# Performance work log

Measured on AMD Instinct MI355X. Metric: run time of the kernel, lower is better.

The kernel has to match this reference:

```python
import jax, jax.numpy as jnp
import numpy as np

EPS = 1e-5
INF = 1e9
H, D = 16, 24  # no_heads, c_hidden

def layer_norm(x, w, b):
    mu = jnp.mean(x, axis=-1, keepdims=True)
    var = jnp.mean(jnp.square(x - mu), axis=-1, keepdims=True)
    return (x - mu) * jax.lax.rsqrt(var + EPS) * w + b

def setup_inputs() -> dict:
    key = jax.random.key(0)
    ks = jax.random.split(key, 12)
    B, N, Cq, Cz = 1, 1024, 384, 128
    s = 0.02
    return {
        "a": jax.random.normal(ks[0], (B, N, Cq), jnp.float32),
        "z": jax.random.normal(ks[1], (B, N, N, Cz), jnp.float32),
        "mask": jnp.ones((B, N), jnp.float32),
        "ln_a_w": jnp.ones((Cq,), jnp.float32),
        "ln_a_b": jnp.zeros((Cq,), jnp.float32),
        "ln_z_w": jnp.ones((Cz,), jnp.float32),
        "ln_z_b": jnp.zeros((Cz,), jnp.float32),
        "w_z": jax.random.normal(ks[2], (Cz, H), jnp.float32) * s,
        "wq": jax.random.normal(ks[3], (Cq, H * D), jnp.float32) * s,
        "wk": jax.random.normal(ks[4], (Cq, H * D), jnp.float32) * s,
        "wv": jax.random.normal(ks[5], (Cq, H * D), jnp.float32) * s,
        "wg": jax.random.normal(ks[6], (Cq, H * D), jnp.float32) * s,
        "bg": jnp.ones((H * D,), jnp.float32),
        "wo": jax.random.normal(ks[7], (H * D, Cq), jnp.float32) * s,
        "bo": jnp.zeros((Cq,), jnp.float32),
    }

def reference(a, z, mask, ln_a_w, ln_a_b, ln_z_w, ln_z_b, w_z, wq, wk, wv, wg, bg, wo, bo):
    B, N, Cq = a.shape
    a_ln = layer_norm(a, ln_a_w, ln_a_b)                      # [B,N,Cq]
    # pair bias: LN -> Linear(no bias) -> permute to [B,H,N,N]
    zb = layer_norm(z, ln_z_w, ln_z_b) @ w_z                  # [B,N,N,H]
    pair_bias = jnp.transpose(zb, (0, 3, 1, 2))               # [B,H,N,N]
    mask_bias = (INF * (mask - 1.0))[:, None, None, :]        # [B,1,1,N]
    q = (a_ln @ wq).reshape(B, N, H, D) * (D ** -0.5)
    k = (a_ln @ wk).reshape(B, N, H, D)
    v = (a_ln @ wv).reshape(B, N, H, D)
    logits = jnp.einsum("bqhd,bkhd->bhqk", q, k) + mask_bias + pair_bias
    attn = jax.nn.softmax(logits, axis=-1)
    o = jnp.einsum("bhqk,bkhd->bqhd", attn, v)                # [B,N,H,D]
    g = jax.nn.sigmoid(a_ln @ wg + bg).reshape(B, N, H, D)
    o = (g * o).reshape(B, N, H * D)
    return o @ wo + bo
```

## Files before the change

### kernel.cpp

```cpp
#include <hip/hip_runtime.h>
#include <hip/hip_bf16.h>

typedef float f32x4 __attribute__((ext_vector_type(4)));
typedef short s16x8 __attribute__((ext_vector_type(8)));

__device__ __forceinline__ unsigned short f2bf(float x){
  unsigned u = __float_as_uint(x);
  u += 0x7fffu + ((u >> 16) & 1u);
  return (unsigned short)(u >> 16);
}
__device__ __forceinline__ float bf2f(unsigned short h){
  return __uint_as_float(((unsigned)h) << 16);
}
__device__ __forceinline__ unsigned pk_bf(float a, float b){
  __hip_bfloat162 t = __float22bfloat162_rn(make_float2(a, b));
  return *reinterpret_cast<unsigned*>(&t);
}

__global__ __launch_bounds__(256) void prep_kernel(const float* __restrict__ a, const float* __restrict__ ln_a_w,
                             const float* __restrict__ ln_a_b, const float* __restrict__ lnzw,
                             const float* __restrict__ lnzb, const float* __restrict__ w_z,
                             const float* __restrict__ wq, const float* __restrict__ wk,
                             const float* __restrict__ wv, const float* __restrict__ wg,
                             const float* __restrict__ wo,
                             unsigned short* __restrict__ a_lnB, unsigned short* __restrict__ wBall,
                             unsigned short* __restrict__ wwB, float* __restrict__ TU,
                             unsigned short* __restrict__ qTp, unsigned short* __restrict__ kTp,
                             unsigned short* __restrict__ vTt){
  int bid = blockIdx.x, tid = threadIdx.x;
  if (bid < 180){
    __shared__ float t[64][65];
    int mat = bid/36, tt = bid - mat*36;
    int c0 = (tt % 6)*64, k0 = (tt / 6)*64;
    const float* src = mat == 0 ? wq : mat == 1 ? wk : mat == 2 ? wv : mat == 3 ? wg : wo;
    int r = tid >> 4, c4 = (tid & 15)*4;
    #pragma unroll
    for (int rr = 0; rr < 4; ++rr){
      float4 v = *(const float4*)(src + (size_t)(k0 + r + rr*16)*384 + c0 + c4);
      t[r + rr*16][c4+0] = v.x; t[r + rr*16][c4+1] = v.y;
      t[r + rr*16][c4+2] = v.z; t[r + rr*16][c4+3] = v.w;
    }
    __syncthreads();
    float scale = (mat == 0) ? 0.20412414523193154f : 1.f;
    int cc = tid >> 2, kp = (tid & 3)*16;
    unsigned ow[8];
    #pragma unroll
    for (int j = 0; j < 8; ++j)
      ow[j] = pk_bf(t[kp + 2*j][cc]*scale, t[kp + 2*j + 1][cc]*scale);
    unsigned short* dst = wBall + ((size_t)(mat*384 + c0 + cc)*384 + k0 + kp);
    *(uint4*)dst       = make_uint4(ow[0], ow[1], ow[2], ow[3]);
    *(uint4*)(dst + 8) = make_uint4(ow[4], ow[5], ow[6], ow[7]);
  } else if (bid < 436){
    int r = (bid - 180)*4 + (tid >> 6), l = tid & 63;
    const float* ap = a + (size_t)r*384;
    float x[6]; float s = 0.f, sq = 0.f;
    #pragma unroll
    for (int i = 0; i < 6; ++i){ x[i] = ap[i*64 + l]; s += x[i]; sq += x[i]*x[i]; }
    #pragma unroll
    for (int off = 32; off; off >>= 1){ s += __shfl_xor(s, off); sq += __shfl_xor(sq, off); }
    float mu = s*(1.f/384.f);
    float var = sq*(1.f/384.f) - mu*mu;
    float rs = rsqrtf(var + 1e-5f);
    #pragma unroll
    for (int i = 0; i < 6; ++i){ int c = i*64 + l; a_lnB[(size_t)r*384 + c] = f2bf((x[i]-mu)*rs*ln_a_w[c] + ln_a_b[c]); }
  } else if (bid == 436){
    if (tid < 128){
      float lw = lnzw[tid];
      #pragma unroll
      for (int h = 0; h < 16; ++h) wwB[tid*16 + h] = f2bf(lw * w_z[tid*16 + h]);
    }
    if (tid < 16){
      float T = 0.f, U = 0.f;
      for (int c = 0; c < 128; ++c){ T += lnzw[c]*w_z[c*16 + tid]; U += lnzb[c]*w_z[c*16 + tid]; }
      TU[tid] = T; TU[16 + tid] = U;
    }
  } else {
    int t = (bid - 437)*256 + tid;
    uint4 zv = make_uint4(0,0,0,0);
    if (t < 16384)      *(uint4*)(qTp + (size_t)t*32 + 24) = zv;
    else if (t < 32768) *(uint4*)(kTp + (size_t)(t - 16384)*32 + 24) = zv;
    else {
      int t2 = t - 32768;
      int h = t2 >> 10, w = t2 & 1023;
      *(uint4*)(vTt + ((size_t)h*32 + 24)*1024 + (size_t)w*8) = zv;
    }
  }
}

__global__ __launch_bounds__(256) void qkvg_kernel(const unsigned short* __restrict__ AB,
                                                   const unsigned short* __restrict__ wBt,
                                                   const float* __restrict__ bg,
                                                   unsigned short* __restrict__ qTp, unsigned short* __restrict__ kTp,
                                                   unsigned short* __restrict__ vTt, float* __restrict__ g){
  __shared__ short Al[64*8*8];
  __shared__ short Bl[64*8*8];
  int tid = threadIdx.x;
  int wave = tid >> 6, lane = tid & 63, l15 = lane & 15, sub = lane >> 4;
  int n0 = blockIdx.x*64, m0 = blockIdx.y*64;
  f32x4 acc[4];
  #pragma unroll
  for (int c = 0; c < 4; ++c) acc[c] = (f32x4){0.f,0.f,0.f,0.f};
  const s16x8* Ag = (const s16x8*)AB;
  const s16x8* Bg = (const s16x8*)wBt;
  s16x8* Al8 = (s16x8*)Al; s16x8* Bl8 = (s16x8*)Bl;
  for (int ks = 0; ks < 6; ++ks){
    int k0u = ks*8;
    #pragma unroll
    for (int j = 0; j < 2; ++j){
      int idx = tid*2 + j;
      int row = idx >> 3, u = idx & 7;
      Al8[row*8 + (u ^ (row & 7))] = Ag[(size_t)(m0 + row)*48 + k0u + u];
      Bl8[row*8 + (u ^ (row & 7))] = Bg[(size_t)(n0 + row)*48 + k0u + u];
    }
    __syncthreads();
    #pragma unroll
    for (int kk = 0; kk < 2; ++kk){
      int arow = wave*16 + l15;
      s16x8 af = Al8[arow*8 + ((kk*4 + sub) ^ (arow & 7))];
      #pragma unroll
      for (int c = 0; c < 4; ++c){
        int brow = c*16 + l15;
        s16x8 bf = Bl8[brow*8 + ((kk*4 + sub) ^ (brow & 7))];
        acc[c] = __builtin_amdgcn_mfma_f32_16x16x32_bf16(af, bf, acc[c], 0, 0, 0);
      }
    }
    __syncthreads();
  }
  int which = blockIdx.x / 6;
  int cb = n0 - which*384;
  if (which == 3){
    #pragma unroll
    for (int c = 0; c < 4; ++c){
      int col = cb + c*16 + l15;
      #pragma unroll
      for (int r = 0; r < 4; ++r){
        int row = m0 + wave*16 + sub*4 + r;
        float t = acc[c][r] + bg[col];
        g[(size_t)row*384 + col] = 1.f/(1.f + __expf(-t));
      }
    }
  } else if (which == 2){
    #pragma unroll
    for (int c = 0; c < 4; ++c){
      int col = cb + c*16 + l15;
      int h = col/24, d = col - h*24;
      unsigned p0 = pk_bf(acc[c][0], acc[c][1]);
      unsigned p1 = pk_bf(acc[c][2], acc[c][3]);
      size_t base = ((size_t)h*32 + d)*1024 + (size_t)(m0 + wave*16 + sub*4);
      *(uint2*)(vTt + base) = make_uint2(p0, p1);
    }
  } else {
    unsigned short* dst = which == 0 ? qTp : kTp;
    #pragma unroll
    for (int c = 0; c < 4; ++c){
      int col = cb + c*16 + l15;
      int h = col/24, d = col - h*24;
      #pragma unroll
      for (int r = 0; r < 4; ++r){
        int row = m0 + wave*16 + sub*4 + r;
        dst[((size_t)(h << 10) + row)*32 + d] = f2bf(acc[c][r]);
      }
    }
  }
}

__global__ __launch_bounds__(256) void zbias_kernel(const float* __restrict__ z, const unsigned short* __restrict__ wwB,
                                                    const float* __restrict__ TU, const float* __restrict__ mask,
                                                    unsigned short* __restrict__ pbM){
  __shared__ float sums[2][64];
  __shared__ float sqs[2][64];
  __shared__ float accT[2][64][17];
  int tid = threadIdx.x;
  int wave = tid >> 6, lane = tid & 63;
  int h = lane & 15, sub = lane >> 4;
  s16x8 bfr[4];
  #pragma unroll
  for (int kc = 0; kc < 4; ++kc)
    #pragma unroll
    for (int j = 0; j < 8; ++j) bfr[kc][j] = (short)wwB[(kc*32 + sub*8 + j)*16 + h];
  s16x8 ones1;
  #pragma unroll
  for (int j = 0; j < 8; ++j) ones1[j] = (h == 0) ? (short)0x3F80 : (short)0;
  int eh = tid >> 4, ej = tid & 15;
  float Te = TU[eh], Ue = TU[16 + eh];
  for (int it = 0; it < 4; ++it){
    int bb = it & 1;
    int tile = blockIdx.x + it*4096;
    int qt = tile >> 6, kt = tile & 63;
    int q0 = qt*4, k0 = kt*16;
    const float* zrow = z + ((size_t)(q0 + wave)*1024 + k0 + h)*128;
    f32x4 acc  = {0.f, 0.f, 0.f, 0.f};
    f32x4 accS = {0.f, 0.f, 0.f, 0.f};
    f32x4 accG = {0.f, 0.f, 0.f, 0.f};
    #pragma unroll
    for (int kc = 0; kc < 4; ++kc){
      f32x4 v0 = *(const f32x4*)(zrow + kc*32 + sub*8);
      f32x4 v1 = *(const f32x4*)(zrow + kc*32 + sub*8 + 4);
      union { unsigned u[4]; s16x8 s; } cv;
      cv.u[0] = pk_bf(v0.x, v0.y); cv.u[1] = pk_bf(v0.z, v0.w);
      cv.u[2] = pk_bf(v1.x, v1.y); cv.u[3] = pk_bf(v1.z, v1.w);
      s16x8 af = cv.s;
      acc  = __builtin_amdgcn_mfma_f32_16x16x32_bf16(af, bfr[kc], acc, 0, 0, 0);
      accS = __builtin_amdgcn_mfma_f32_16x16x32_bf16(af, ones1, accS, 0, 0, 0);
      accG = __builtin_amdgcn_mfma_f32_16x16x32_bf16(af, af, accG, 0, 0, 0);
    }
    #pragma unroll
    for (int r = 0; r < 4; ++r) accT[bb][wave*16 + sub*4 + r][h] = acc[r];
    if (h == 0){
      #pragma unroll
      for (int r = 0; r < 4; ++r) sums[bb][wave*16 + sub*4 + r] = accS[r];
    }
    if (sub == (h >> 2)){
      int r = h & 3;
      float vq = r == 0 ? accG[0] : r == 1 ? accG[1] : r == 2 ? accG[2] : accG[3];
      sqs[bb][wave*16 + h] = vq;
    }
    __syncthreads();
    int k = k0 + ej;
    float mb = 1e9f*(mask[k] - 1.f);
    unsigned short pv[4];
    #pragma unroll
    for (int i = 0; i < 4; ++i){
      int row = i*16 + ej;
      float mu = sums[bb][row]*(1.f/128.f);
      float var = sqs[bb][row]*(1.f/128.f) - mu*mu;
      float rs = rsqrtf(var + 1e-5f);
      pv[i] = f2bf(rs*(accT[bb][row][eh] - mu*Te) + Ue + mb);
    }
    int qb = q0 >> 6, qg = (q0 >> 4) & 3, subq = (q0 >> 2) & 3;
    int kkt = k >> 6, c = (k >> 4) & 3, l15k = k & 15;
    size_t off = ((((size_t)(eh*16 + qb)*16 + kkt)*4 + qg)*4 + c)*256 + (size_t)(subq*16 + l15k)*4;
    *(uint2*)(pbM + off) = make_uint2(((unsigned)pv[1] << 16) | pv[0], ((unsigned)pv[3] << 16) | pv[2]);
  }
}

__global__ __launch_bounds__(512) void attn_kernel(const unsigned short* __restrict__ qTp, const unsigned short* __restrict__ kTp,
                                                   const unsigned short* __restrict__ vTt, const unsigned short* __restrict__ pbM,
                                                   const float* __restrict__ g, unsigned short* __restrict__ ogB){
  __shared__ float lds[8192];
  int tid = threadIdx.x;
  int wave = tid >> 6, lane = tid & 63, l15 = lane & 15, sub = lane >> 4;
  int qb32 = blockIdx.x, h = blockIdx.y;
  int qg_l = wave & 1, kkq = wave >> 1;
  int qrow = qb32*32 + qg_l*16 + l15;
  int qb64 = qb32 >> 1, qg4 = (qb32 & 1)*2 + qg_l;
  const unsigned short* kBase = kTp + ((size_t)(h << 10))*32;
  const unsigned short* vBase = vTt + (size_t)h*32*1024;
  const unsigned short* pbW = pbM + (size_t)(h*16 + qb64)*16*4096 + (size_t)qg4*1024 + (size_t)lane*4;
  uint2 pvAll[4][4];
  #pragma unroll
  for (int t = 0; t < 4; ++t){
    const unsigned short* pbt = pbW + (size_t)(kkq*4 + t)*4096;
    pvAll[t][0] = *(const uint2*)(pbt + 0);
    pvAll[t][1] = *(const uint2*)(pbt + 256);
    pvAll[t][2] = *(const uint2*)(pbt + 512);
    pvAll[t][3] = *(const uint2*)(pbt + 768);
  }
  s16x8 qf = *(const s16x8*)(qTp + ((size_t)(h << 10) + qrow)*32 + sub*8);
  f32x4 o0 = {0.f,0.f,0.f,0.f}, o1 = {0.f,0.f,0.f,0.f};
  float m[4] = {-1e30f,-1e30f,-1e30f,-1e30f}, l[4] = {0.f,0.f,0.f,0.f};
  char* Pb = (char*)(lds + wave*1024);
  s16x8 kfA0, kfA1, kfA2, kfA3;
  {
    int kk0 = (kkq*4)*64;
    kfA0 = *(const s16x8*)(kBase + (size_t)(kk0 +  0 + l15)*32 + sub*8);
    kfA1 = *(const s16x8*)(kBase + (size_t)(kk0 + 16 + l15)*32 + sub*8);
    kfA2 = *(const s16x8*)(kBase + (size_t)(kk0 + 32 + l15)*32 + sub*8);
    kfA3 = *(const s16x8*)(kBase + (size_t)(kk0 + 48 + l15)*32 + sub*8);
  }
  #pragma unroll
  for (int t = 0; t < 4; ++t){
    int kkt = kkq*4 + t;
    int kk0 = kkt*64;
    f32x4 s[4];
    s[0] = __builtin_amdgcn_mfma_f32_16x16x32_bf16(qf, kfA0, (f32x4){0.f,0.f,0.f,0.f}, 0, 0, 0);
    s[1] = __builtin_amdgcn_mfma_f32_16x16x32_bf16(qf, kfA1, (f32x4){0.f,0.f,0.f,0.f}, 0, 0, 0);
    s[2] = __builtin_amdgcn_mfma_f32_16x16x32_bf16(qf, kfA2, (f32x4){0.f,0.f,0.f,0.f}, 0, 0, 0);
    s[3] = __builtin_amdgcn_mfma_f32_16x16x32_bf16(qf, kfA3, (f32x4){0.f,0.f,0.f,0.f}, 0, 0, 0);
    if (t < 3){
      int nk = kk0 + 64;
      kfA0 = *(const s16x8*)(kBase + (size_t)(nk +  0 + l15)*32 + sub*8);
      kfA1 = *(const s16x8*)(kBase + (size_t)(nk + 16 + l15)*32 + sub*8);
      kfA2 = *(const s16x8*)(kBase + (size_t)(nk + 32 + l15)*32 + sub*8);
      kfA3 = *(const s16x8*)(kBase + (size_t)(nk + 48 + l15)*32 + sub*8);
    }
    #pragma unroll
    for (int c = 0; c < 4; ++c){
      s[c][0] += bf2f((unsigned short)(pvAll[t][c].x & 0xffff));
      s[c][1] += bf2f((unsigned short)(pvAll[t][c].x >> 16));
      s[c][2] += bf2f((unsigned short)(pvAll[t][c].y & 0xffff));
      s[c][3] += bf2f((unsigned short)(pvAll[t][c].y >> 16));
    }
    #pragma unroll
    for (int r = 0; r < 4; ++r){
      float pm = fmaxf(fmaxf(s[0][r], s[1][r]), fmaxf(s[2][r], s[3][r]));
      pm = fmaxf(pm, __shfl_xor(pm, 1));
      pm = fmaxf(pm, __shfl_xor(pm, 2));
      pm = fmaxf(pm, __shfl_xor(pm, 4));
      pm = fmaxf(pm, __shfl_xor(pm, 8));
      float mn = fmaxf(m[r], pm);
      float corr = __expf(m[r] - mn);
      m[r] = mn;
      float ps = 0.f;
      #pragma unroll
      for (int c = 0; c < 4; ++c){ s[c][r] = __expf(s[c][r] - mn); ps += s[c][r]; }
      ps += __shfl_xor(ps, 1); ps += __shfl_xor(ps, 2);
      ps += __shfl_xor(ps, 4); ps += __shfl_xor(ps, 8);
      l[r] = l[r]*corr + ps;
      o0[r] *= corr; o1[r] *= corr;
    }
    #pragma unroll
    for (int c = 0; c < 4; ++c){
      #pragma unroll
      for (int r = 0; r < 4; ++r){
        int qq = sub*4 + r;
        int byte = ((qq*128 + (c*16 + l15)*2)) ^ ((qq & 7) << 4);
        *(short*)(Pb + byte) = (short)f2bf(s[c][r]);
      }
    }
    #pragma unroll
    for (int kh = 0; kh < 2; ++kh){
      int byteA = (l15*128 + kh*64 + sub*16) ^ ((l15 & 7) << 4);
      s16x8 pa = *(const s16x8*)(Pb + byteA);
      s16x8 vb0 = *(const s16x8*)(vBase + (size_t)l15*1024 + kk0 + kh*32 + sub*8);
      s16x8 vb1 = *(const s16x8*)(vBase + (size_t)(16 + l15)*1024 + kk0 + kh*32 + sub*8);
      o0 = __builtin_amdgcn_mfma_f32_16x16x32_bf16(pa, vb0, o0, 0, 0, 0);
      o1 = __builtin_amdgcn_mfma_f32_16x16x32_bf16(pa, vb1, o1, 0, 0, 0);
    }
  }
  {
    float* cw = lds + wave*1024 + lane*16;
    cw[0] = o0[0]; cw[1] = o0[1]; cw[2] = o0[2]; cw[3] = o0[3];
    cw[4] = o1[0]; cw[5] = o1[1]; cw[6] = o1[2]; cw[7] = o1[3];
    cw[8] = m[0]; cw[9] = m[1]; cw[10] = m[2]; cw[11] = m[3];
    cw[12] = l[0]; cw[13] = l[1]; cw[14] = l[2]; cw[15] = l[3];
  }
  __syncthreads();
  if (kkq == 0){
    #pragma unroll
    for (int k2 = 1; k2 < 4; ++k2){
      const float* c2 = lds + (size_t)(k2*2 + qg_l)*1024 + lane*16;
      #pragma unroll
      for (int r = 0; r < 4; ++r){
        float m2 = c2[8 + r], l2 = c2[12 + r];
        float nm = fmaxf(m[r], m2);
        float f1 = __expf(m[r] - nm), f2 = __expf(m2 - nm);
        l[r] = l[r]*f1 + l2*f2;
        o0[r] = o0[r]*f1 + c2[r]*f2;
        o1[r] = o1[r]*f1 + c2[4 + r]*f2;
        m[r] = nm;
      }
    }
    #pragma unroll
    for (int r = 0; r < 4; ++r){
      float inv = 1.f/l[r];
      int q = qb32*32 + qg_l*16 + sub*4 + r;
      size_t base = (size_t)q*384 + h*24;
      ogB[base + l15] = f2bf(g[base + l15]*o0[r]*inv);
      if (l15 < 8) ogB[base + 16 + l15] = f2bf(g[base + 16 + l15]*o1[r]*inv);
    }
  }
}

__global__ __launch_bounds__(256) void gemm_out(const unsigned short* __restrict__ AB,
                                                const unsigned short* __restrict__ wBo,
                                                const float* __restrict__ bo, float* __restrict__ dst){
  __shared__ short Al[64*8*8];
  __shared__ short Bl[64*8*8];
  int tid = threadIdx.x;
  int wave = tid >> 6, lane = tid & 63, l15 = lane & 15, sub = lane >> 4;
  int n0 = blockIdx.x*64, m0 = blockIdx.y*64;
  f32x4 acc[4];
  #pragma unroll
  for (int c = 0; c < 4; ++c) acc[c] = (f32x4){0.f,0.f,0.f,0.f};
  const s16x8* Ag = (const s16x8*)AB;
  const s16x8* Bg = (const s16x8*)wBo;
  s16x8* Al8 = (s16x8*)Al; s16x8* Bl8 = (s16x8*)Bl;
  for (int ks = 0; ks < 6; ++ks){
    int k0u = ks*8;
    #pragma unroll
    for (int j = 0; j < 2; ++j){
      int idx = tid*2 + j;
      int row = idx >> 3, u = idx & 7;
      Al8[row*8 + (u ^ (row & 7))] = Ag[(size_t)(m0 + row)*48 + k0u + u];
      Bl8[row*8 + (u ^ (row & 7))] = Bg[(size_t)(n0 + row)*48 + k0u + u];
    }
    __syncthreads();
    #pragma unroll
    for (int kk = 0; kk < 2; ++kk){
      int arow = wave*16 + l15;
      s16x8 af = Al8[arow*8 + ((kk*4 + sub) ^ (arow & 7))];
      #pragma unroll
      for (int c = 0; c < 4; ++c){
        int brow = c*16 + l15;
        s16x8 bf = Bl8[brow*8 + ((kk*4 + sub) ^ (brow & 7))];
        acc[c] = __builtin_amdgcn_mfma_f32_16x16x32_bf16(af, bf, acc[c], 0, 0, 0);
      }
    }
    __syncthreads();
  }
  #pragma unroll
  for (int c = 0; c < 4; ++c){
    int col = n0 + c*16 + l15;
    float b = bo[col];
    #pragma unroll
    for (int r = 0; r < 4; ++r){
      int row = m0 + wave*16 + sub*4 + r;
      dst[(size_t)row*384 + col] = acc[c][r] + b;
    }
  }
}

extern "C" void kernel_launch(void* const* d_in, const int* in_sizes, int n_in,
                              void* d_out, int out_size, void* d_ws, size_t ws_size,
                              hipStream_t stream){
  const float* a      = (const float*)d_in[0];
  const float* z      = (const float*)d_in[1];
  const float* mask   = (const float*)d_in[2];
  const float* ln_a_w = (const float*)d_in[3];
  const float* ln_a_b = (const float*)d_in[4];
  const float* ln_z_w = (const float*)d_in[5];
  const float* ln_z_b = (const float*)d_in[6];
  const float* w_z    = (const float*)d_in[7];
  const float* wq     = (const float*)d_in[8];
  const float* wk     = (const float*)d_in[9];
  const float* wv     = (const float*)d_in[10];
  const float* wg     = (const float*)d_in[11];
  const float* bg     = (const float*)d_in[12];
  const float* wo     = (const float*)d_in[13];
  const float* bo     = (const float*)d_in[14];

  char* ws = (char*)d_ws;
  unsigned short* a_lnB = (unsigned short*)(ws + ((size_t)0u));
  unsigned short* wBall = (unsigned short*)(ws + ((size_t)1u << 20));
  unsigned short* qTp   = (unsigned short*)(ws + ((size_t)4u << 20));
  unsigned short* kTp   = (unsigned short*)(ws + ((size_t)6u << 20));
  unsigned short* vTt   = (unsigned short*)(ws + ((size_t)8u << 20));
  float* g    = (float*)(ws + ((size_t)10u << 20));
  unsigned short* ogB = (unsigned short*)(ws + ((size_t)12u << 20));
  unsigned short* wwB = (unsigned short*)(ws + ((size_t)14u << 20));
  float* TU   = (float*)(ws + ((size_t)14u << 20) + 8192);
  unsigned short* pbM = (unsigned short*)(ws + ((size_t)24u << 20));

  hipLaunchKernelGGL(prep_kernel, dim3(629), dim3(256), 0, stream, a, ln_a_w, ln_a_b,
                     ln_z_w, ln_z_b, w_z, wq, wk, wv, wg, wo, a_lnB, wBall, wwB, TU, qTp, kTp, vTt);
  hipLaunchKernelGGL(qkvg_kernel, dim3(24,16), dim3(256), 0, stream, a_lnB, wBall, bg, qTp, kTp, vTt, g);
  hipLaunchKernelGGL(zbias_kernel, dim3(4096), dim3(256), 0, stream, z, wwB, TU, mask, pbM);
  hipLaunchKernelGGL(attn_kernel, dim3(32,16), dim3(512), 0, stream, qTp, kTp, vTt, pbM, g, ogB);
  hipLaunchKernelGGL(gemm_out, dim3(6,16), dim3(256), 0, stream, ogB, wBall + (size_t)4*384*384, bo, (float*)d_out);
}
```

Baseline: 159.0 us.

## Transpose QK^T MFMA so softmax rows lie along lanes, retile pair-bias layout

The attention kernel swaps the MFMA operands so each lane holds scores for a single query across keys. The row max and sum then need only two cross-lane shuffles instead of four per row, and the P tile is written to LDS as packed 8-byte stores rather than individual shorts. The pair-bias kernel is retiled (16 queries x 4 keys per tile) and the pbM layout is changed to match the new score fragment ordering, so the bias is still read with coalesced uint2 loads. The cost is extra __shfl broadcasts to move per-row correction factors into the output accumulator layout, plus a riskier change in index mapping across two kernels.

```diff
diff --git a/kernel.cpp b/kernel.cpp
--- a/kernel.cpp
+++ b/kernel.cpp
@@ -181,14 +181,16 @@
   s16x8 ones1;
   #pragma unroll
   for (int j = 0; j < 8; ++j) ones1[j] = (h == 0) ? (short)0x3F80 : (short)0;
-  int eh = tid >> 4, ej = tid & 15;
+  int eh = tid >> 4, eq = tid & 15;
   float Te = TU[eh], Ue = TU[16 + eh];
+  uint2* pbU = (uint2*)pbM;
+  int row_l = wave*16 + h;
   for (int it = 0; it < 4; ++it){
     int bb = it & 1;
     int tile = blockIdx.x + it*4096;
-    int qt = tile >> 6, kt = tile & 63;
-    int q0 = qt*4, k0 = kt*16;
-    const float* zrow = z + ((size_t)(q0 + wave)*1024 + k0 + h)*128;
+    int qt = tile >> 8, kt = tile & 255;
+    int q0 = qt*16, k0 = kt*4;
+    const float* zrow = z + ((size_t)(q0 + (row_l >> 2))*1024 + k0 + (row_l & 3))*128;
     f32x4 acc  = {0.f, 0.f, 0.f, 0.f};
     f32x4 accS = {0.f, 0.f, 0.f, 0.f};
     f32x4 accG = {0.f, 0.f, 0.f, 0.f};
@@ -216,21 +218,24 @@
       sqs[bb][wave*16 + h] = vq;
     }
     __syncthreads();
-    int k = k0 + ej;
-    float mb = 1e9f*(mask[k] - 1.f);
+    float4 mk = *(const float4*)(mask + k0);
+    float mbv0 = 1e9f*(mk.x - 1.f), mbv1 = 1e9f*(mk.y - 1.f);
+    float mbv2 = 1e9f*(mk.z - 1.f), mbv3 = 1e9f*(mk.w - 1.f);
     unsigned short pv[4];
     #pragma unroll
-    for (int i = 0; i < 4; ++i){
-      int row = i*16 + ej;
+    for (int kl = 0; kl < 4; ++kl){
+      int row = eq*4 + kl;
       float mu = sums[bb][row]*(1.f/128.f);
       float var = sqs[bb][row]*(1.f/128.f) - mu*mu;
       float rs = rsqrtf(var + 1e-5f);
-      pv[i] = f2bf(rs*(accT[bb][row][eh] - mu*Te) + Ue + mb);
-    }
-    int qb = q0 >> 6, qg = (q0 >> 4) & 3, subq = (q0 >> 2) & 3;
-    int kkt = k >> 6, c = (k >> 4) & 3, l15k = k & 15;
-    size_t off = ((((size_t)(eh*16 + qb)*16 + kkt)*4 + qg)*4 + c)*256 + (size_t)(subq*16 + l15k)*4;
-    *(uint2*)(pbM + off) = make_uint2(((unsigned)pv[1] << 16) | pv[0], ((unsigned)pv[3] << 16) | pv[2]);
+      float mb = kl == 0 ? mbv0 : kl == 1 ? mbv1 : kl == 2 ? mbv2 : mbv3;
+      pv[kl] = f2bf(rs*(accT[bb][row][eh] - mu*Te) + Ue + mb);
+    }
+    int q = q0 + eq;
+    int qb = q >> 6, qg = (q >> 4) & 3, l15q = q & 15;
+    int kkt = k0 >> 6, c = (k0 >> 4) & 3, subk = (k0 >> 2) & 3;
+    pbU[((((size_t)(eh*16 + qb)*16 + kkt)*4 + qg)*4 + c)*64 + subk*16 + l15q] =
+        make_uint2(((unsigned)pv[1] << 16) | pv[0], ((unsigned)pv[3] << 16) | pv[2]);
   }
 }
 
@@ -246,19 +251,19 @@
   int qb64 = qb32 >> 1, qg4 = (qb32 & 1)*2 + qg_l;
   const unsigned short* kBase = kTp + ((size_t)(h << 10))*32;
   const unsigned short* vBase = vTt + (size_t)h*32*1024;
-  const unsigned short* pbW = pbM + (size_t)(h*16 + qb64)*16*4096 + (size_t)qg4*1024 + (size_t)lane*4;
+  const uint2* pbU = (const uint2*)pbM;
   uint2 pvAll[4][4];
   #pragma unroll
   for (int t = 0; t < 4; ++t){
-    const unsigned short* pbt = pbW + (size_t)(kkq*4 + t)*4096;
-    pvAll[t][0] = *(const uint2*)(pbt + 0);
-    pvAll[t][1] = *(const uint2*)(pbt + 256);
-    pvAll[t][2] = *(const uint2*)(pbt + 512);
-    pvAll[t][3] = *(const uint2*)(pbt + 768);
+    size_t tb = ((((size_t)(h*16 + qb64)*16 + (kkq*4 + t))*4 + qg4)*4)*64 + lane;
+    pvAll[t][0] = pbU[tb +   0];
+    pvAll[t][1] = pbU[tb +  64];
+    pvAll[t][2] = pbU[tb + 128];
+    pvAll[t][3] = pbU[tb + 192];
   }
   s16x8 qf = *(const s16x8*)(qTp + ((size_t)(h << 10) + qrow)*32 + sub*8);
   f32x4 o0 = {0.f,0.f,0.f,0.f}, o1 = {0.f,0.f,0.f,0.f};
-  float m[4] = {-1e30f,-1e30f,-1e30f,-1e30f}, l[4] = {0.f,0.f,0.f,0.f};
+  float m = -1e30f, lsum = 0.f;
   char* Pb = (char*)(lds + wave*1024);
   s16x8 kfA0, kfA1, kfA2, kfA3;
   {
@@ -270,13 +275,12 @@
   }
   #pragma unroll
   for (int t = 0; t < 4; ++t){
-    int kkt = kkq*4 + t;
-    int kk0 = kkt*64;
+    int kk0 = (kkq*4 + t)*64;
     f32x4 s[4];
-    s[0] = __builtin_amdgcn_mfma_f32_16x16x32_bf16(qf, kfA0, (f32x4){0.f,0.f,0.f,0.f}, 0, 0, 0);
-    s[1] = __builtin_amdgcn_mfma_f32_16x16x32_bf16(qf, kfA1, (f32x4){0.f,0.f,0.f,0.f}, 0, 0, 0);
-    s[2] = __builtin_amdgcn_mfma_f32_16x16x32_bf16(qf, kfA2, (f32x4){0.f,0.f,0.f,0.f}, 0, 0, 0);
-    s[3] = __builtin_amdgcn_mfma_f32_16x16x32_bf16(qf, kfA3, (f32x4){0.f,0.f,0.f,0.f}, 0, 0, 0);
+    s[0] = __builtin_amdgcn_mfma_f32_16x16x32_bf16(kfA0, qf, (f32x4){0.f,0.f,0.f,0.f}, 0, 0, 0);
+    s[1] = __builtin_amdgcn_mfma_f32_16x16x32_bf16(kfA1, qf, (f32x4){0.f,0.f,0.f,0.f}, 0, 0, 0);
+    s[2] = __builtin_amdgcn_mfma_f32_16x16x32_bf16(kfA2, qf, (f32x4){0.f,0.f,0.f,0.f}, 0, 0, 0);
+    s[3] = __builtin_amdgcn_mfma_f32_16x16x32_bf16(kfA3, qf, (f32x4){0.f,0.f,0.f,0.f}, 0, 0, 0);
     if (t < 3){
       int nk = kk0 + 64;
       kfA0 = *(const s16x8*)(kBase + (size_t)(nk +  0 + l15)*32 + sub*8);
@@ -291,32 +295,37 @@
       s[c][2] += bf2f((unsigned short)(pvAll[t][c].y & 0xffff));
       s[c][3] += bf2f((unsigned short)(pvAll[t][c].y >> 16));
     }
-    #pragma unroll
-    for (int r = 0; r < 4; ++r){
-      float pm = fmaxf(fmaxf(s[0][r], s[1][r]), fmaxf(s[2][r], s[3][r]));
-      pm = fmaxf(pm, __shfl_xor(pm, 1));
-      pm = fmaxf(pm, __shfl_xor(pm, 2));
-      pm = fmaxf(pm, __shfl_xor(pm, 4));
-      pm = fmaxf(pm, __shfl_xor(pm, 8));
-      float mn = fmaxf(m[r], pm);
-      float corr = __expf(m[r] - mn);
-      m[r] = mn;
-      float ps = 0.f;
-      #pragma unroll
-      for (int c = 0; c < 4; ++c){ s[c][r] = __expf(s[c][r] - mn); ps += s[c][r]; }
-      ps += __shfl_xor(ps, 1); ps += __shfl_xor(ps, 2);
-      ps += __shfl_xor(ps, 4); ps += __shfl_xor(ps, 8);
-      l[r] = l[r]*corr + ps;
-      o0[r] *= corr; o1[r] *= corr;
-    }
-    #pragma unroll
-    for (int c = 0; c < 4; ++c){
-      #pragma unroll
-      for (int r = 0; r < 4; ++r){
-        int qq = sub*4 + r;
-        int byte = ((qq*128 + (c*16 + l15)*2)) ^ ((qq & 7) << 4);
-        *(short*)(Pb + byte) = (short)f2bf(s[c][r]);
-      }
+    float p01 = fmaxf(fmaxf(s[0][0], s[0][1]), fmaxf(s[0][2], s[0][3]));
+    float p23 = fmaxf(fmaxf(s[1][0], s[1][1]), fmaxf(s[1][2], s[1][3]));
+    float p45 = fmaxf(fmaxf(s[2][0], s[2][1]), fmaxf(s[2][2], s[2][3]));
+    float p67 = fmaxf(fmaxf(s[3][0], s[3][1]), fmaxf(s[3][2], s[3][3]));
+    float pm = fmaxf(fmaxf(p01, p23), fmaxf(p45, p67));
+    pm = fmaxf(pm, __shfl_xor(pm, 16));
+    pm = fmaxf(pm, __shfl_xor(pm, 32));
+    float mn = fmaxf(m, pm);
+    float corrL = __expf(m - mn);
+    m = mn;
+    float ps = 0.f;
+    #pragma unroll
+    for (int c = 0; c < 4; ++c){
+      #pragma unroll
+      for (int r = 0; r < 4; ++r){ s[c][r] = __expf(s[c][r] - mn); ps += s[c][r]; }
+    }
+    ps += __shfl_xor(ps, 16);
+    ps += __shfl_xor(ps, 32);
+    lsum = lsum*corrL + ps;
+    float cr0 = __shfl(corrL, sub*4 + 0);
+    float cr1 = __shfl(corrL, sub*4 + 1);
+    float cr2 = __shfl(corrL, sub*4 + 2);
+    float cr3 = __shfl(corrL, sub*4 + 3);
+    o0[0] *= cr0; o0[1] *= cr1; o0[2] *= cr2; o0[3] *= cr3;
+    o1[0] *= cr0; o1[1] *= cr1; o1[2] *= cr2; o1[3] *= cr3;
+    #pragma unroll
+    for (int c = 0; c < 4; ++c){
+      unsigned u0 = pk_bf(s[c][0], s[c][1]);
+      unsigned u1 = pk_bf(s[c][2], s[c][3]);
+      int byte = (l15*128 + c*32 + sub*8) ^ ((l15 & 7) << 4);
+      *(uint2*)(Pb + byte) = make_uint2(u0, u1);
     }
     #pragma unroll
     for (int kh = 0; kh < 2; ++kh){
@@ -328,12 +337,18 @@
       o1 = __builtin_amdgcn_mfma_f32_16x16x32_bf16(pa, vb1, o1, 0, 0, 0);
     }
   }
+  float mr[4], lr[4];
+  #pragma unroll
+  for (int r = 0; r < 4; ++r){
+    mr[r] = __shfl(m, sub*4 + r);
+    lr[r] = __shfl(lsum, sub*4 + r);
+  }
   {
     float* cw = lds + wave*1024 + lane*16;
     cw[0] = o0[0]; cw[1] = o0[1]; cw[2] = o0[2]; cw[3] = o0[3];
     cw[4] = o1[0]; cw[5] = o1[1]; cw[6] = o1[2]; cw[7] = o1[3];
-    cw[8] = m[0]; cw[9] = m[1]; cw[10] = m[2]; cw[11] = m[3];
-    cw[12] = l[0]; cw[13] = l[1]; cw[14] = l[2]; cw[15] = l[3];
+    cw[8] = mr[0]; cw[9] = mr[1]; cw[10] = mr[2]; cw[11] = mr[3];
+    cw[12] = lr[0]; cw[13] = lr[1]; cw[14] = lr[2]; cw[15] = lr[3];
   }
   __syncthreads();
   if (kkq == 0){
@@ -343,17 +358,17 @@
       #pragma unroll
       for (int r = 0; r < 4; ++r){
         float m2 = c2[8 + r], l2 = c2[12 + r];
-        float nm = fmaxf(m[r], m2);
-        float f1 = __expf(m[r] - nm), f2 = __expf(m2 - nm);
-        l[r] = l[r]*f1 + l2*f2;
+        float nm = fmaxf(mr[r], m2);
+        float f1 = __expf(mr[r] - nm), f2 = __expf(m2 - nm);
+        lr[r] = lr[r]*f1 + l2*f2;
         o0[r] = o0[r]*f1 + c2[r]*f2;
         o1[r] = o1[r]*f1 + c2[4 + r]*f2;
-        m[r] = nm;
+        mr[r] = nm;
       }
     }
     #pragma unroll
     for (int r = 0; r < 4; ++r){
-      float inv = 1.f/l[r];
+      float inv = 1.f/lr[r];
       int q = qb32*32 + qg_l*16 + sub*4 + r;
       size_t base = (size_t)q*384 + h*24;
       ogB[base + l15] = f2bf(g[base + l15]*o0[r]*inv);
```

After: 156.3 us, median of 2. Within noise of the previous version (-1.7%).
